# Kernel optimization log

Measured on AMD Instinct MI355X. Metric: run time of the kernel, lower is better.

## Reference

```python
import jax, jax.numpy as jnp
import numpy as np

B, N, E = 16, 512, 131072
FEAT, EMB, H = 3, 512, 3
K1, K2 = 410, 205  # ceil(0.8*512), ceil(0.5*410) per PyG TopKPooling
NEG_SLOPE, EPS = 0.2, 1e-5


def _gat_conv(x, W, att_s, att_d, bias, src, tgt, valid, num_nodes):
    # PyG GATConv (concat=True): per-edge attention with segment softmax over targets.
    Hh, C = att_s.shape
    xp = (x @ W).reshape(-1, Hh, C)                      # [Nn,H,C]
    a_s = jnp.einsum('nhc,hc->nh', xp, att_s)
    a_d = jnp.einsum('nhc,hc->nh', xp, att_d)
    srcc = jnp.where(valid, src, 0)
    tgtc = jnp.where(valid, tgt, 0)
    e = jax.nn.leaky_relu(a_s[srcc] + a_d[tgtc], NEG_SLOPE)  # [Ee,H]
    seg = jnp.where(valid, tgt, num_nodes)               # invalid edges -> dummy segment
    emax = jax.ops.segment_max(e, seg, num_segments=num_nodes + 1)
    emax = jnp.where(jnp.isfinite(emax), emax, 0.0)
    ex = jnp.exp(e - emax[seg]) * valid[:, None].astype(e.dtype)
    den = jax.ops.segment_sum(ex, seg, num_segments=num_nodes + 1)
    alpha = ex / jnp.maximum(den[seg], 1e-16)            # [Ee,H]
    out = jax.ops.segment_sum(alpha[:, :, None] * xp[srcc], seg,
                              num_segments=num_nodes + 1)[:num_nodes]
    return out.reshape(num_nodes, Hh * C) + bias


def _bn(x, g, b):
    # BatchNorm1d, training-mode batch statistics (biased var), eps=1e-5
    m = x.mean(0)
    v = x.var(0)
    return (x - m) * jax.lax.rsqrt(v + EPS) * g + b


def _topk_pool(x, p, nb, n_per, k):
    # PyG TopKPooling: score = tanh(x.w/||w||), keep top-k per graph, scale by score
    score = jnp.tanh((x @ p) / jnp.linalg.norm(p))       # [nb*n_per]
    top_s, top_i = jax.lax.top_k(score.reshape(nb, n_per), k)
    perm = (top_i + jnp.arange(nb)[:, None] * n_per).reshape(-1)
    x_new = x[perm] * top_s.reshape(-1, 1)
    mapping = jnp.full((nb * n_per,), -1, jnp.int32).at[perm].set(
        jnp.arange(nb * k, dtype=jnp.int32))
    return x_new, mapping


def _pool_cat(x, nb, k):
    # [global_max_pool, global_mean_pool] over equal-size graphs
    xr = x.reshape(nb, k, -1)
    return jnp.concatenate([xr.max(1), xr.mean(1)], axis=1)


def _forward(x, W1, as1, ad1, bc1, Wh1, bh1, g1, be1, p1,
             W2, as2, ad2, bc2, Wh2, bh2, g2, be2, p2,
             Wl1, bl1, Wl2, bl2, edge_index):
    Nn = B * N
    src0, tgt0 = edge_index[0], edge_index[1]
    sl = jnp.arange(Nn, dtype=jnp.int32)                 # GATConv add_self_loops=True
    src1 = jnp.concatenate([src0, sl]); tgt1 = jnp.concatenate([tgt0, sl])
    valid1 = jnp.ones(src1.shape, bool)
    h = _gat_conv(x, W1, as1, ad1, bc1, src1, tgt1, valid1, Nn)
    h = jax.nn.relu(h @ Wh1 + bh1)
    h = _bn(h, g1, be1)
    h, mapping = _topk_pool(h, p1, B, N, K1)
    x1 = _pool_cat(h, B, K1)                             # [B, 2*EMB]
    # relabel edges to pooled node ids; drop edges with removed endpoints via mask
    s2 = mapping[src0]; t2 = mapping[tgt0]
    v2 = (s2 >= 0) & (t2 >= 0)
    sl2 = jnp.arange(B * K1, dtype=jnp.int32)
    src2 = jnp.concatenate([s2, sl2]); tgt2 = jnp.concatenate([t2, sl2])
    valid2 = jnp.concatenate([v2, jnp.ones(sl2.shape, bool)])
    h = _gat_conv(h, W2, as2, ad2, bc2, src2, tgt2, valid2, B * K1)
    h = jax.nn.relu(h @ Wh2 + bh2)
    h = _bn(h, g2, be2)
    h, _ = _topk_pool(h, p2, B, K1, K2)
    x2 = _pool_cat(h, B, K2)
    xg = x1 + x2
    xg = jax.nn.relu(xg @ Wl1 + bl1)                     # dropout p=0.5 disabled (eval)
    return xg @ Wl2 + bl2                                # [B, 256]


def setup_inputs() -> dict:
    key = jax.random.key(0)
    ks = jax.random.split(key, 16)
    x = jax.random.normal(ks[0], (B * N, FEAT), jnp.float32)
    goff = jnp.repeat(jnp.arange(B, dtype=jnp.int32), E // B) * N
    src = jax.random.randint(ks[1], (E,), 0, N, jnp.int32) + goff
    tgt = jax.random.randint(ks[2], (E,), 0, N, jnp.int32) + goff
    edge_index = jnp.stack([src, tgt])
    s = 0.05
    p = {
        'W1': jax.random.normal(ks[3], (FEAT, H * EMB)) * s,
        'as1': jax.random.normal(ks[4], (H, EMB)) * s,
        'ad1': jax.random.normal(ks[5], (H, EMB)) * s,
        'bc1': jnp.zeros((H * EMB,)),
        'Wh1': jax.random.normal(ks[6], (H * EMB, EMB)) * s,
        'bh1': jnp.zeros((EMB,)),
        'g1': jnp.ones((EMB,)), 'be1': jnp.zeros((EMB,)),
        'p1': jax.random.normal(ks[7], (EMB,)) * s,
        'W2': jax.random.normal(ks[8], (EMB, H * EMB)) * s,
        'as2': jax.random.normal(ks[9], (H, EMB)) * s,
        'ad2': jax.random.normal(ks[10], (H, EMB)) * s,
        'bc2': jnp.zeros((H * EMB,)),
        'Wh2': jax.random.normal(ks[11], (H * EMB, EMB)) * s,
        'bh2': jnp.zeros((EMB,)),
        'g2': jnp.ones((EMB,)), 'be2': jnp.zeros((EMB,)),
        'p2': jax.random.normal(ks[12], (EMB,)) * s,
        'Wl1': jax.random.normal(ks[13], (2 * EMB, 512)) * s,
        'bl1': jnp.zeros((512,)),
        'Wl2': jax.random.normal(ks[14], (512, 256)) * s,
        'bl2': jnp.zeros((256,)),
    }
    return {'x': x, 'edge_index': edge_index, **p}


def reference(x, edge_index, W1, as1, ad1, bc1, Wh1, bh1, g1, be1, p1,
              W2, as2, ad2, bc2, Wh2, bh2, g2, be2, p2, Wl1, bl1, Wl2, bl2):
    return _forward(x, W1, as1, ad1, bc1, Wh1, bh1, g1, be1, p1,
                    W2, as2, ad2, bc2, Wh2, bh2, g2, be2, p2,
                    Wl1, bl1, Wl2, bl2, edge_index)
```

## Files before the change

kernel.cpp:

```cpp
#include <hip/hip_runtime.h>
#include <hip/hip_bf16.h>
#include <math.h>

#define E_EDGES 131072
#define NN1 8192
#define NN2 6560
#define NG 16
#define NP1 512
#define KP1 410
#define KP2 205
#define F1 1536
#define EMB 512
#define MAXDEG 256

typedef __hip_bfloat16 bf16;
typedef __attribute__((ext_vector_type(8))) short short8;
typedef __attribute__((ext_vector_type(4))) float f32x4;
typedef __attribute__((ext_vector_type(4))) unsigned short us4;

__device__ inline float wred64(float v){
  #pragma unroll
  for (int o = 32; o; o >>= 1) v += __shfl_down(v, o);
  return v;
}
__device__ inline float b2f_raw(unsigned short u){
  return __uint_as_float((unsigned)u << 16);
}
union BFU { bf16 b; unsigned short u; };
__device__ inline unsigned short f2u(float v){ BFU x; x.b = __float2bfloat16(v); return x.u; }

__device__ __forceinline__ void gld16(const void* g, void* l){
  __builtin_amdgcn_global_load_lds(
      (const __attribute__((address_space(1))) void*)g,
      (__attribute__((address_space(3))) void*)l, 16, 0, 0);
}

__device__ inline void split_store(float v, bf16* __restrict__ ph, bf16* __restrict__ pl){
  bf16 hi = __float2bfloat16(v);
  *ph = hi;
  *pl = __float2bfloat16(v - __bfloat162float(hi));
}

__device__ inline void bn_from_acc(const float* __restrict__ bnacc, int c, float fM,
                                   float& mean, float& inv){
  mean = bnacc[c] / fM;
  float var = fmaxf(bnacc[512+c]/fM - mean*mean, 0.f);
  inv = 1.f / sqrtf(var + 1e-5f);
}

__global__ __launch_bounds__(256) void k_pre(
    const float* __restrict__ W1, const float* __restrict__ as1, const float* __restrict__ ad1,
    const float* __restrict__ Wh1, const float* __restrict__ bc1, const float* __restrict__ bh1,
    const float* __restrict__ W2, const float* __restrict__ as2, const float* __restrict__ ad2,
    const float* __restrict__ Wh2, const float* __restrict__ bc2, const float* __restrict__ bh2,
    const int* __restrict__ src0, const int* __restrict__ tgt0, const float* __restrict__ x,
    float* __restrict__ M1p, float* __restrict__ cvp,
    float* __restrict__ was2, float* __restrict__ wad2,
    float* __restrict__ Zb, int* __restrict__ cnt2, int* __restrict__ map,
    bf16* __restrict__ Th, bf16* __restrict__ Tl,
    float* __restrict__ denp, float* __restrict__ nump){
  int b = blockIdx.x, t = threadIdx.x;
  if (b < 24){
    int h = b / 8, rem = b % 8, jh = rem >> 2, kc = rem & 3;
    int j = jh*256 + t, c0 = kc*128;
    __shared__ float w1s[3][128];
    for (int i = t; i < 384; i += 256)
      w1s[i>>7][i&127] = W1[(i>>7)*1536 + h*512 + c0 + (i&127)];
    __syncthreads();
    const float* whc = Wh1 + (size_t)(h*512 + c0)*512 + j;
    float a0=0.f, a1=0.f, a2=0.f;
    #pragma unroll 8
    for (int c = 0; c < 128; c++){
      float v = whc[(size_t)c*512];
      a0 += w1s[0][c]*v; a1 += w1s[1][c]*v; a2 += w1s[2][c]*v;
    }
    float* dst = M1p + (size_t)kc*4608;
    dst[(h*3+0)*512 + j] = a0;
    dst[(h*3+1)*512 + j] = a1;
    dst[(h*3+2)*512 + j] = a2;
  } else if (b < 56){
    int b2 = b - 24;
    int which = b2 >> 4, rem = b2 & 15, jh = rem >> 3, kc = rem & 7;
    const float* bc = which ? bc2 : bc1;
    const float* Wh = which ? Wh2 : Wh1;
    const float* bh = which ? bh2 : bh1;
    int j = jh*256 + t, i0 = kc*192;
    float acc = (kc == 0) ? bh[j] : 0.f;
    #pragma unroll 8
    for (int i = 0; i < 192; i++)
      acc += bc[i0+i] * Wh[(size_t)(i0+i)*512 + j];
    cvp[(size_t)(which*8 + kc)*512 + j] = acc;
  } else if (b < 152){
    int b3 = b - 56;
    int y = b3 >> 4, et = b3 & 15;
    int kind = y / 3, h = y % 3;
    int w = t >> 6, lane = t & 63;
    const float* att = kind ? ad2 : as2;
    float a[8];
    #pragma unroll
    for (int u = 0; u < 8; u++) a[u] = att[h*512 + lane*8 + u];
    for (int r = w; r < 32; r += 4){
      int e = et*32 + r;
      const float4* row = (const float4*)(W2 + (size_t)e*1536 + h*512) + lane*2;
      float4 v0 = row[0], v1 = row[1];
      float d = v0.x*a[0]+v0.y*a[1]+v0.z*a[2]+v0.w*a[3]
              + v1.x*a[4]+v1.y*a[5]+v1.z*a[6]+v1.w*a[7];
      d = wred64(d);
      if (lane == 0) (kind ? wad2 : was2)[h*512 + e] = d;
    }
  } else if (b < 218){
    int i = (b - 152)*256 + t;
    if (i < 2048){ Zb[i] = 0.f; }
    else if (i < 2048 + NN2){ cnt2[i - 2048] = 1; }
    else if (i < 2048 + NN2 + NN1){ map[i - 2048 - NN2] = -1; }
  } else if (b < 474){
    __shared__ float sww[18];
    __shared__ float lden[1536];
    __shared__ float lnum[4608];
    int wv_ = t >> 6, lane = t & 63;
    for (int combo = wv_*5; combo < wv_*5+5 && combo < 18; combo++){
      int kind = combo/9, rr = combo%9, h = rr/3, f = rr%3;
      const float* att = kind ? ad1 : as1;
      float s = 0.f;
      #pragma unroll
      for (int c = lane; c < 512; c += 64) s += W1[f*1536 + h*512 + c] * att[h*512 + c];
      s = wred64(s);
      if (lane == 0) sww[combo] = s;
    }
    for (int i = t; i < 1536; i += 256) lden[i] = 0.f;
    for (int i = t; i < 4608; i += 256) lnum[i] = 0.f;
    __syncthreads();
    int eb = b - 218;
    int g = eb >> 4, ch = eb & 15;
    int base = g*8192;
    int it0 = ch*544;
    for (int k = t; k < 544; k += 256){
      int it = it0 + k;
      int s, tl;
      if (it < 8192){ s = src0[base+it]; tl = tgt0[base+it] & 511; }
      else { tl = it - 8192; s = g*512 + tl; }
      float xs0 = x[s*3], xs1 = x[s*3+1], xs2 = x[s*3+2];
      int tg = g*512 + tl;
      float xt0 = x[tg*3], xt1 = x[tg*3+1], xt2 = x[tg*3+2];
      #pragma unroll
      for (int h = 0; h < 3; h++){
        float v = xs0*sww[h*3]+xs1*sww[h*3+1]+xs2*sww[h*3+2]
                + xt0*sww[9+h*3]+xt1*sww[9+h*3+1]+xt2*sww[9+h*3+2];
        v = v > 0.f ? v : 0.2f*v;
        float pe = expf(v);
        atomicAdd(&lden[tl*3 + h], pe);
        atomicAdd(&lnum[tl*9 + h*3 + 0], pe * xs0);
        atomicAdd(&lnum[tl*9 + h*3 + 1], pe * xs1);
        atomicAdd(&lnum[tl*9 + h*3 + 2], pe * xs2);
      }
    }
    __syncthreads();
    for (int i = t; i < 4608; i += 256) nump[(size_t)eb*4608 + i] = lnum[i];
    for (int i = t; i < 1536; i += 256) denp[(size_t)eb*1536 + i] = lden[i];
  } else {
    int bb = b - 474;
    int z = bb % 3; int rr = bb / 3; int by = rr >> 3, bx = rr & 7;
    const float* A = W2 + (size_t)z*512;
    const float* B = Wh2 + (size_t)z*512*512;
    __shared__ __align__(16) short sAh[4096], sAl[4096], sBh[4096], sBl[4096];
    int w = t >> 6, lane = t & 63;
    int l16 = lane & 15, q = lane >> 4;
    int bm = by*64, bn = bx*64;
    int am  = t >> 2, akw = (t & 3)*16;
    int bnl = t & 63, bkq = (t >> 6)*16;
    f32x4 acc[4];
    #pragma unroll
    for (int nf = 0; nf < 4; nf++) acc[nf] = (f32x4){0.f,0.f,0.f,0.f};
    float va[16], vb[16];
    #define GS_LOAD(K0) do { \
      _Pragma("unroll") for (int u = 0; u < 4; u++){ \
        float4 v4 = *(const float4*)(A + (size_t)(bm+am)*1536 + (K0) + akw + u*4); \
        va[u*4]=v4.x; va[u*4+1]=v4.y; va[u*4+2]=v4.z; va[u*4+3]=v4.w; } \
      _Pragma("unroll") for (int u = 0; u < 16; u++) \
        vb[u] = B[(size_t)((K0) + bkq + u)*512 + bn + bnl]; \
    } while(0)
    GS_LOAD(0);
    for (int it = 0; it < 8; it++){
      #pragma unroll
      for (int hh = 0; hh < 2; hh++){
        short8 ah_, al_, bh_, bl_;
        #pragma unroll
        for (int jj = 0; jj < 8; jj++){
          float v = va[hh*8+jj];
          unsigned short hu = f2u(v);
          ah_[jj] = (short)hu; al_[jj] = (short)f2u(v - b2f_raw(hu));
          v = vb[hh*8+jj];
          hu = f2u(v);
          bh_[jj] = (short)hu; bl_[jj] = (short)f2u(v - b2f_raw(hu));
        }
        int aoff = am*64  + ((((akw>>3) + hh) ^ (am  & 7)) << 3);
        *(short8*)(sAh + aoff) = ah_;
        *(short8*)(sAl + aoff) = al_;
        int boff = bnl*64 + ((((bkq>>3) + hh) ^ (bnl & 7)) << 3);
        *(short8*)(sBh + boff) = bh_;
        *(short8*)(sBl + boff) = bl_;
      }
      __syncthreads();
      if (it < 7) GS_LOAD((it+1)*64);
      #pragma unroll
      for (int ks = 0; ks < 2; ks++){
        int gc = ks*4 + q;
        int ar = w*16 + l16;
        int ao = ar*64 + ((gc ^ (ar & 7)) << 3);
        short8 afh = *(const short8*)(sAh + ao);
        short8 afl = *(const short8*)(sAl + ao);
        #pragma unroll
        for (int nf = 0; nf < 4; nf++){
          int br = nf*16 + l16;
          int bo = br*64 + ((gc ^ (br & 7)) << 3);
          short8 bfh = *(const short8*)(sBh + bo);
          short8 bfl = *(const short8*)(sBl + bo);
          acc[nf] = __builtin_amdgcn_mfma_f32_16x16x32_bf16(afh, bfh, acc[nf], 0, 0, 0);
          acc[nf] = __builtin_amdgcn_mfma_f32_16x16x32_bf16(afh, bfl, acc[nf], 0, 0, 0);
          acc[nf] = __builtin_amdgcn_mfma_f32_16x16x32_bf16(afl, bfh, acc[nf], 0, 0, 0);
        }
      }
      __syncthreads();
    }
    #undef GS_LOAD
    int m0 = bm + w*16 + q*4;
    #pragma unroll
    for (int nf = 0; nf < 4; nf++){
      int n = bn + nf*16 + l16;
      size_t base = (size_t)n*1536 + (size_t)z*512 + m0;
      #pragma unroll
      for (int e = 0; e < 4; e++)
        split_store(acc[nf][e], &Th[base+e], &Tl[base+e]);
    }
  }
}

__global__ __launch_bounds__(256) void k_h1(
    const float* __restrict__ nump, const float* __restrict__ denp,
    const float* __restrict__ M1p, const float* __restrict__ cvp1, bf16* __restrict__ hout,
    float* __restrict__ bnacc1){
  __shared__ float sM[9*512];
  __shared__ float sC[512];
  __shared__ float sA[32*9];
  int t = threadIdx.x; int n0 = blockIdx.x*32;
  for (int i = t; i < 9*512; i += 256)
    sM[i] = M1p[i] + M1p[4608 + i] + M1p[2*4608 + i] + M1p[3*4608 + i];
  for (int i = t; i < 512; i += 256){
    float s = 0.f;
    #pragma unroll
    for (int kc = 0; kc < 8; kc++) s += cvp1[kc*512 + i];
    sC[i] = s;
  }
  for (int i = t; i < 288; i += 256){
    int node = i / 9, q = i % 9, hh = q / 3;
    int gn = n0 + node;
    int g = gn >> 9, nl = gn & 511;
    float ns = 0.f, ds = 0.f;
    #pragma unroll 4
    for (int ch = 0; ch < 16; ch++){
      ns += nump[(size_t)(g*16 + ch)*4608 + nl*9 + q];
      ds += denp[(size_t)(g*16 + ch)*1536 + nl*3 + hh];
    }
    sA[i] = ns / fmaxf(ds, 1e-16f);
  }
  __syncthreads();
  float c0v = sC[t], c1v = sC[t+256];
  float ls0=0.f, lq0=0.f, ls1=0.f, lq1=0.f;
  #pragma unroll 4
  for (int i = 0; i < 32; i++){
    float a0 = c0v, a1 = c1v;
    #pragma unroll
    for (int q = 0; q < 9; q++){
      float av = sA[i*9+q];
      a0 += av * sM[q*512 + t];
      a1 += av * sM[q*512 + t + 256];
    }
    a0 = fmaxf(a0, 0.f); a1 = fmaxf(a1, 0.f);
    hout[(size_t)(n0+i)*512 + t]       = __float2bfloat16(a0);
    hout[(size_t)(n0+i)*512 + t + 256] = __float2bfloat16(a1);
    ls0 += a0; lq0 += a0*a0; ls1 += a1; lq1 += a1*a1;
  }
  atomicAdd(&bnacc1[t],           ls0);
  atomicAdd(&bnacc1[t+256],       ls1);
  atomicAdd(&bnacc1[512 + t],     lq0);
  atomicAdd(&bnacc1[512 + t+256], lq1);
}

__global__ __launch_bounds__(256) void k_score(
    const bf16* __restrict__ h, const float* __restrict__ bnacc, int M,
    const float* __restrict__ g_, const float* __restrict__ be, const float* __restrict__ p,
    float* __restrict__ score, int NR){
  __shared__ float w[512];
  __shared__ float rb[4], rp[4];
  int t = threadIdx.x;
  int lane = t & 63, wv = t >> 6;
  float fM = (float)M;
  float bt = 0.f, pp = 0.f;
  #pragma unroll
  for (int k = 0; k < 2; k++){
    int c = t + k*256;
    float mean, inv; bn_from_acc(bnacc, c, fM, mean, inv);
    float gc = g_[c], pc = p[c];
    float ig = inv * gc;
    w[c] = ig * pc;
    bt += (be[c] - mean * ig) * pc;
    pp += pc * pc;
  }
  bt = wred64(bt); pp = wred64(pp);
  if (lane == 0){ rb[wv] = bt; rp[wv] = pp; }
  __syncthreads();
  float B0 = rb[0]+rb[1]+rb[2]+rb[3];
  float pn = sqrtf(rp[0]+rp[1]+rp[2]+rp[3]);
  float wl[8];
  #pragma unroll
  for (int u = 0; u < 8; u++) wl[u] = w[lane*8 + u];
  int rbase = blockIdx.x*32 + wv*8;
  for (int rr = 0; rr < 8; rr++){
    int r = rbase + rr;
    if (r >= NR) break;
    const unsigned short* hr = (const unsigned short*)h + (size_t)r*EMB + lane*8;
    us4 v0 = *(const us4*)(hr);
    us4 v1 = *(const us4*)(hr + 4);
    float dot = b2f_raw(v0.x)*wl[0] + b2f_raw(v0.y)*wl[1]
              + b2f_raw(v0.z)*wl[2] + b2f_raw(v0.w)*wl[3]
              + b2f_raw(v1.x)*wl[4] + b2f_raw(v1.y)*wl[5]
              + b2f_raw(v1.z)*wl[6] + b2f_raw(v1.w)*wl[7];
    dot = wred64(dot);
    if (lane == 0) score[r] = tanhf((dot + B0) / pn);
  }
}

__global__ __launch_bounds__(512) void k_sort1(
    const float* __restrict__ score, int n_per, int K,
    int* __restrict__ map, int* __restrict__ topi, float* __restrict__ tops){
  int g = blockIdx.x, t = threadIdx.x;
  __shared__ float sk[512];
  __shared__ int si[512];
  if (t < n_per){ sk[t] = score[g*n_per + t]; si[t] = t; }
  else { sk[t] = -INFINITY; si[t] = 0x7fffffff; }
  __syncthreads();
  for (int k = 2; k <= 512; k <<= 1){
    for (int j = k >> 1; j > 0; j >>= 1){
      int l = t ^ j;
      if (l > t){
        float ki = sk[t], kl = sk[l]; int ii = si[t], il = si[l];
        bool before_l = (kl > ki) || (kl == ki && il < ii);
        bool up = ((t & k) == 0);
        if (up == before_l){ sk[t]=kl; sk[l]=ki; si[t]=il; si[l]=ii; }
      }
      __syncthreads();
    }
  }
  if (t < K){
    map[g*n_per + si[t]] = g*K + t;
    topi[g*K + t] = si[t];
    tops[g*K + t] = sk[t];
  }
}

__global__ __launch_bounds__(512) void k_sortpool2(
    const bf16* __restrict__ h, const float* __restrict__ score,
    const float* __restrict__ bnacc, int M,
    const float* __restrict__ g_, const float* __restrict__ be,
    int n_per, int K, float* __restrict__ cat){
  int g = blockIdx.x, t = threadIdx.x;
  __shared__ float sk[512];
  __shared__ int si[512];
  if (t < n_per){ sk[t] = score[g*n_per + t]; si[t] = t; }
  else { sk[t] = -INFINITY; si[t] = 0x7fffffff; }
  __syncthreads();
  for (int k = 2; k <= 512; k <<= 1){
    for (int j = k >> 1; j > 0; j >>= 1){
      int l = t ^ j;
      if (l > t){
        float ki = sk[t], kl = sk[l]; int ii = si[t], il = si[l];
        bool before_l = (kl > ki) || (kl == ki && il < ii);
        bool up = ((t & k) == 0);
        if (up == before_l){ sk[t]=kl; sk[l]=ki; si[t]=il; si[l]=ii; }
      }
      __syncthreads();
    }
  }
  float fM = (float)M;
  float mean, inv; bn_from_acc(bnacc, t, fM, mean, inv);
  float ig = inv * g_[t], bec = be[t];
  const unsigned short* hp = (const unsigned short*)h;
  float mx = -INFINITY, sm = 0.f;
  for (int r = 0; r < K; r++){
    float v = (b2f_raw(hp[(size_t)(g*n_per + si[r])*EMB + t]) - mean) * ig + bec;
    v *= sk[r];
    mx = fmaxf(mx, v); sm += v;
  }
  cat[g*1024 + t] = mx;
  cat[g*1024 + 512 + t] = sm / (float)K;
}

__global__ __launch_bounds__(256) void k_gather_c2(
    const bf16* __restrict__ h, const float* __restrict__ bnacc, int M,
    const float* __restrict__ gm, const float* __restrict__ be,
    const int* __restrict__ topi, const float* __restrict__ tops,
    bf16* __restrict__ xn, int n_per, int K,
    const float* __restrict__ was2, const float* __restrict__ wad2,
    float* __restrict__ aso, float* __restrict__ ado,
    const int* __restrict__ src0, const int* __restrict__ tgt0,
    const int* __restrict__ map, int* __restrict__ cnt2, int nblk_g){
  int row = blockIdx.x, t = threadIdx.x;
  if (row >= nblk_g){
    int i = (row - nblk_g)*256 + t;
    if (i < E_EDGES){
      int s = map[src0[i]], tg = map[tgt0[i]];
      if (s >= 0 && tg >= 0) atomicAdd(&cnt2[tg], 1);
    }
    return;
  }
  int gr = row / K, i = row - gr*K;
  int sidx = topi[gr*K + i];
  float s = tops[gr*K + i];
  const bf16* src = h + ((size_t)(gr*n_per + sidx))*EMB;
  bf16* dst = xn + (size_t)row*EMB;
  int c0 = t, c1 = t + 256;
  float fM = (float)M;
  float mean0, inv0, mean1, inv1;
  bn_from_acc(bnacc, c0, fM, mean0, inv0);
  bn_from_acc(bnacc, c1, fM, mean1, inv1);
  float v0 = ((__bfloat162float(src[c0]) - mean0) * inv0 * gm[c0] + be[c0]) * s;
  float v1 = ((__bfloat162float(src[c1]) - mean1) * inv1 * gm[c1] + be[c1]) * s;
  dst[c0] = __float2bfloat16(v0);
  dst[c1] = __float2bfloat16(v1);
  {
    float a[6];
    #pragma unroll
    for (int hh = 0; hh < 3; hh++){
      a[hh]   = v0*was2[hh*512 + c0] + v1*was2[hh*512 + c1];
      a[3+hh] = v0*wad2[hh*512 + c0] + v1*wad2[hh*512 + c1];
    }
    __shared__ float red[6][4];
    int lane = t & 63, wv = t >> 6;
    #pragma unroll
    for (int q = 0; q < 6; q++){ float v = wred64(a[q]); if (lane==0) red[q][wv]=v; }
    __syncthreads();
    if (t < 6){
      float sm = red[t][0]+red[t][1]+red[t][2]+red[t][3];
      if (t < 3) aso[row*3+t] = sm; else ado[row*3+(t-3)] = sm;
    }
  }
}

__device__ inline void scan_body(const int* __restrict__ counts, int* __restrict__ off,
                                 int* __restrict__ cur, int n, int* __restrict__ sh){
  int t = threadIdx.x;
  int chunk = (n + 1023) >> 10;
  int b = t * chunk; int e = b + chunk; if (e > n) e = n;
  int s = 0;
  for (int i = b; i < e; i++) s += counts[i];
  sh[t] = s; __syncthreads();
  for (int o = 1; o < 1024; o <<= 1){
    int v = (t >= o) ? sh[t-o] : 0;
    __syncthreads();
    sh[t] += v;
    __syncthreads();
  }
  int run = (t > 0) ? sh[t-1] : 0;
  for (int i = b; i < e; i++){ int c = counts[i]; off[i] = run; cur[i] = run; run += c; }
  if (t == 1023) off[n] = sh[1023];
}
__global__ void k_fill2(const int* __restrict__ src0, const int* __restrict__ tgt0,
                        const int* __restrict__ map, int* __restrict__ cur,
                        int* __restrict__ esrc, int E, int nn){
  int i = blockIdx.x*blockDim.x + threadIdx.x;
  if (i >= E + nn) return;
  int s, tg;
  if (i < E){
    s = map[src0[i]]; tg = map[tgt0[i]];
    if (s < 0 || tg < 0) return;
  } else { s = i - E; tg = s; }
  int pos = atomicAdd(&cur[tg], 1);
  esrc[pos] = s;
}

__global__ __launch_bounds__(1024) void k_poolA_scan(const bf16* __restrict__ xn,
    float* __restrict__ cat, int K,
    const int* __restrict__ cnt2, int* __restrict__ off2, int* __restrict__ cur2){
  __shared__ int shi[1024];
  __shared__ float smax[8][128];
  __shared__ float ssum[8][128];
  int b = blockIdx.x, t = threadIdx.x;
  if (b == 64){ scan_body(cnt2, off2, cur2, NN2, shi); return; }
  int g = b >> 2, cb = b & 3;
  int c = t & 127, rg = t >> 7;
  int col = cb*128 + c;
  const unsigned short* p = (const unsigned short*)xn + (size_t)g*K*EMB + col;
  float mx = -INFINITY, sm = 0.f;
  for (int r = rg; r < K; r += 8){
    float v = b2f_raw(p[(size_t)r*EMB]);
    mx = fmaxf(mx, v); sm += v;
  }
  smax[rg][c] = mx; ssum[rg][c] = sm;
  __syncthreads();
  if (rg == 0){
    #pragma unroll
    for (int u = 1; u < 8; u++){ mx = fmaxf(mx, smax[u][c]); sm += ssum[u][c]; }
    cat[g*1024 + col] = mx;
    cat[g*1024 + 512 + col] = sm / (float)K;
  }
}

__global__ __launch_bounds__(256) void k_agg2(
    const bf16* __restrict__ xn, const float* __restrict__ aso, const float* __restrict__ ado,
    const int* __restrict__ off, const int* __restrict__ esrc,
    bf16* __restrict__ oh){
  int n = blockIdx.x, t = threadIdx.x;
  __shared__ int srcs[MAXDEG];
  __shared__ float al[MAXDEG*3];
  __shared__ float mh[3], dh[3];
  int s0 = off[n]; int deg = off[n+1] - s0; if (deg > MAXDEG) deg = MAXDEG;
  for (int e = t; e < deg; e += 256) srcs[e] = esrc[s0 + e];
  __syncthreads();
  float ad0 = ado[n*3+0], ad1 = ado[n*3+1], ad2 = ado[n*3+2];
  for (int e = t; e < deg; e += 256){
    int s = srcs[e];
    float v0 = aso[s*3+0] + ad0, v1 = aso[s*3+1] + ad1, v2 = aso[s*3+2] + ad2;
    al[e*3+0] = v0 > 0.f ? v0 : 0.2f*v0;
    al[e*3+1] = v1 > 0.f ? v1 : 0.2f*v1;
    al[e*3+2] = v2 > 0.f ? v2 : 0.2f*v2;
  }
  __syncthreads();
  if (t < 3){
    float m = -INFINITY;
    for (int e = 0; e < deg; e++) m = fmaxf(m, al[e*3+t]);
    float d = 0.f;
    for (int e = 0; e < deg; e++) d += expf(al[e*3+t] - m);
    mh[t] = m; dh[t] = 1.f / fmaxf(d, 1e-16f);
  }
  __syncthreads();
  for (int e = t; e < deg; e += 256){
    al[e*3+0] = expf(al[e*3+0]-mh[0])*dh[0];
    al[e*3+1] = expf(al[e*3+1]-mh[1])*dh[1];
    al[e*3+2] = expf(al[e*3+2]-mh[2])*dh[2];
  }
  __syncthreads();
  float acc[2][3] = {};
  for (int e = 0; e < deg; e++){
    int s = srcs[e];
    float a0 = al[e*3], a1 = al[e*3+1], a2 = al[e*3+2];
    #pragma unroll
    for (int k = 0; k < 2; k++){
      float v = __bfloat162float(xn[(size_t)s*512 + t + k*256]);
      acc[k][0] += a0*v; acc[k][1] += a1*v; acc[k][2] += a2*v;
    }
  }
  #pragma unroll
  for (int k = 0; k < 2; k++){
    int c = t + k*256;
    #pragma unroll
    for (int h = 0; h < 3; h++)
      oh[(size_t)n*1536 + h*512 + c] = __float2bfloat16(acc[k][h]);
  }
}

__global__ __launch_bounds__(256, 2) void k_gemm_mfma(
    const bf16* __restrict__ Ah,
    const bf16* __restrict__ Bh, const bf16* __restrict__ Bl,
    const float* __restrict__ bias, bf16* __restrict__ C,
    float* __restrict__ bnacc,
    int M, int N, int K, int Mtiles){
  int xcd = (int)blockIdx.x & 7;
  int ii  = (int)blockIdx.x >> 3;
  int bni = ii & 7;
  int bmi = xcd + 8*(ii >> 3);
  if (bmi >= Mtiles) return;
  __shared__ __align__(16) unsigned short lds[2][16384];
  int t = threadIdx.x, w = t >> 6, lane = t & 63;
  int q = lane >> 4, l16 = lane & 15;
  int bm = bmi * 128, bn = bni * 64;

  int lr = lane >> 3, lc = lane & 7;
  int kg = ((lc ^ lr) & 7) * 8;
  int ro = w*8 + lr;
  int m0 = bm + ro, m1 = bm + 32 + ro, m2 = bm + 64 + ro, m3 = bm + 96 + ro;
  if (m0 >= M) m0 = M-1;  if (m1 >= M) m1 = M-1;
  if (m2 >= M) m2 = M-1;  if (m3 >= M) m3 = M-1;
  int n0 = bn + ro, n1 = bn + 32 + ro;
  const bf16* ptr[8];
  ptr[0] = Ah + (size_t)m0*K + kg;
  ptr[1] = Ah + (size_t)m1*K + kg;
  ptr[2] = Ah + (size_t)m2*K + kg;
  ptr[3] = Ah + (size_t)m3*K + kg;
  ptr[4] = Bh + (size_t)n0*K + kg;
  ptr[5] = Bh + (size_t)n1*K + kg;
  ptr[6] = Bl + (size_t)n0*K + kg;
  ptr[7] = Bl + (size_t)n1*K + kg;
  const int dof[8] = {0, 2048, 4096, 6144, 8192, 10240, 12288, 14336};

  int wm = (w >> 1) * 64, wn = (w & 1) * 32;
  f32x4 acc[4][2];
  #pragma unroll
  for (int i = 0; i < 4; i++)
    #pragma unroll
    for (int j = 0; j < 2; j++)
      acc[i][j] = (f32x4){0.f, 0.f, 0.f, 0.f};

  #pragma unroll
  for (int u = 0; u < 8; u++){
    gld16(ptr[u], &lds[0][dof[u] + w*512]);
    ptr[u] += 64;
  }

  int nit = K >> 6;
  for (int it = 0; it < nit; it++){
    __syncthreads();
    int cur = it & 1;
    if (it + 1 < nit){
      int nxt = cur ^ 1;
      #pragma unroll
      for (int u = 0; u < 8; u++){
        gld16(ptr[u], &lds[nxt][dof[u] + w*512]);
        ptr[u] += 64;
      }
    }
    const unsigned short* L = lds[cur];
    #pragma unroll
    for (int ks = 0; ks < 2; ks++){
      short8 ah[4], bh2[2], bl2[2];
      int gc = ks*4 + q;
      #pragma unroll
      for (int i = 0; i < 4; i++){
        int r = wm + i*16 + l16;
        ah[i] = *(const short8*)(L + r*64 + ((gc ^ (r & 7)) << 3));
      }
      #pragma unroll
      for (int j = 0; j < 2; j++){
        int r = wn + j*16 + l16;
        int so = ((gc ^ (r & 7)) << 3);
        bh2[j] = *(const short8*)(L + 8192  + r*64 + so);
        bl2[j] = *(const short8*)(L + 12288 + r*64 + so);
      }
      #pragma unroll
      for (int i = 0; i < 4; i++)
        #pragma unroll
        for (int j = 0; j < 2; j++){
          acc[i][j] = __builtin_amdgcn_mfma_f32_16x16x32_bf16(ah[i], bh2[j], acc[i][j], 0, 0, 0);
          acc[i][j] = __builtin_amdgcn_mfma_f32_16x16x32_bf16(ah[i], bl2[j], acc[i][j], 0, 0, 0);
        }
    }
  }

  __syncthreads();
  float* cs = (float*)&lds[0][0];
  float* cq = cs + 128;
  int slot = w >> 1;
  #pragma unroll
  for (int j = 0; j < 2; j++){
    int c_local = wn + j*16 + l16;
    int c = bn + c_local;
    float bv = 0.f;
    if (bias){
      #pragma unroll
      for (int kc = 0; kc < 8; kc++) bv += bias[kc*512 + c];
    }
    float ls = 0.f, lq = 0.f;
    #pragma unroll
    for (int i = 0; i < 4; i++){
      int rb = bm + wm + i*16 + q*4;
      #pragma unroll
      for (int e = 0; e < 4; e++){
        int r = rb + e;
        if (r < M){
          float v = fmaxf(acc[i][j][e] + bv, 0.f);
          C[(size_t)r*N + c] = __float2bfloat16(v);
          ls += v; lq += v*v;
        }
      }
    }
    ls += __shfl_xor(ls, 16); ls += __shfl_xor(ls, 32);
    lq += __shfl_xor(lq, 16); lq += __shfl_xor(lq, 32);
    if (q == 0){ cs[slot*64 + c_local] = ls; cq[slot*64 + c_local] = lq; }
  }
  __syncthreads();
  if (t < 64){
    atomicAdd(&bnacc[bn + t],        cs[t] + cs[64 + t]);
    atomicAdd(&bnacc[512 + bn + t],  cq[t] + cq[64 + t]);
  }
}

__global__ __launch_bounds__(256) void k_head1p(const float* __restrict__ c1,
    const float* __restrict__ c2, const float* __restrict__ Wl1,
    float* __restrict__ t1p){
  __shared__ float wl[128][64];
  __shared__ float xgs[16][128];
  int b = blockIdx.x, t = threadIdx.x;
  int jt = b >> 3, kc = b & 7;
  int j0 = jt*64, k0 = kc*128;
  for (int i = t; i < 8192; i += 256){
    int k = i >> 6, j = i & 63;
    wl[k][j] = Wl1[(size_t)(k0 + k)*512 + j0 + j];
  }
  for (int i = t; i < 2048; i += 256){
    int g = i >> 7, k = i & 127;
    int idx = g*1024 + k0 + k;
    xgs[g][k] = c1[idx] + c2[idx];
  }
  __syncthreads();
  #pragma unroll
  for (int u = 0; u < 4; u++){
    int p = t + u*256;
    int g = p >> 6, j = p & 63;
    float acc = 0.f;
    #pragma unroll 8
    for (int k = 0; k < 128; k++)
      acc += xgs[g][k] * wl[k][j];
    t1p[(size_t)(kc*16 + g)*512 + j0 + j] = acc;
  }
}
__global__ __launch_bounds__(512) void k_head2p(const float* __restrict__ t1p,
    const float* __restrict__ bl1, const float* __restrict__ Wl2,
    const float* __restrict__ bl2, float* __restrict__ out){
  __shared__ float t1s[512];
  __shared__ float part[2][256];
  int g = blockIdx.x, t = threadIdx.x;
  float acc = bl1[t];
  #pragma unroll
  for (int kc = 0; kc < 8; kc++)
    acc += t1p[(size_t)(kc*16 + g)*512 + t];
  t1s[t] = fmaxf(acc, 0.f);
  __syncthreads();
  int c = t & 255, half = t >> 8;
  float a = 0.f;
  #pragma unroll 8
  for (int k = half*256; k < half*256 + 256; k++)
    a += t1s[k] * Wl2[(size_t)k*256 + c];
  part[half][c] = a;
  __syncthreads();
  if (half == 0)
    out[g*256 + c] = part[0][c] + part[1][c] + bl2[c];
}

extern "C" void kernel_launch(void* const* d_in, const int* in_sizes, int n_in,
                              void* d_out, int out_size, void* d_ws, size_t ws_size,
                              hipStream_t stream){
  const float* x   = (const float*)d_in[0];
  const int*   ei  = (const int*)d_in[1];
  const float* W1  = (const float*)d_in[2];
  const float* as1 = (const float*)d_in[3];
  const float* ad1 = (const float*)d_in[4];
  const float* bc1 = (const float*)d_in[5];
  const float* Wh1 = (const float*)d_in[6];
  const float* bh1 = (const float*)d_in[7];
  const float* g1  = (const float*)d_in[8];
  const float* be1 = (const float*)d_in[9];
  const float* p1  = (const float*)d_in[10];
  const float* W2  = (const float*)d_in[11];
  const float* as2 = (const float*)d_in[12];
  const float* ad2 = (const float*)d_in[13];
  const float* bc2 = (const float*)d_in[14];
  const float* Wh2 = (const float*)d_in[15];
  const float* bh2 = (const float*)d_in[16];
  const float* g2  = (const float*)d_in[17];
  const float* be2 = (const float*)d_in[18];
  const float* p2  = (const float*)d_in[19];
  const float* Wl1 = (const float*)d_in[20];
  const float* bl1 = (const float*)d_in[21];
  const float* Wl2 = (const float*)d_in[22];
  const float* bl2 = (const float*)d_in[23];
  float* out = (float*)d_out;

  const int* src0 = ei;
  const int* tgt0 = ei + E_EDGES;

  bf16* Cc      = (bf16*)d_ws;
  bf16* xn1     = Cc + (size_t)NN1*EMB;
  bf16* aggx2h  = xn1 + (size_t)NN2*EMB;
  bf16* M2Th    = aggx2h + (size_t)NN2*F1;
  bf16* M2Tl    = M2Th + (size_t)EMB*F1;
  float* holeA  = (float*)(M2Tl + (size_t)EMB*F1);
  float* t1p    = holeA;
  float* score  = holeA + 65536;
  float* bnacc1 = holeA + 122880;
  float* bnacc  = bnacc1 + 1024;
  float* M1p    = bnacc + 1024;
  float* cvp    = M1p + 4*4608;
  float* was2   = cvp + 16*512;
  float* wad2   = was2 + 3*512;
  float* hole16 = wad2 + 3*512;
  float* aso2   = hole16 + 32;
  float* ado2   = aso2 + (size_t)NN2*3;
  float* tops   = ado2 + (size_t)NN2*3;
  float* cat1   = tops + NG*KP1;
  float* cat2   = cat1 + NG*1024;
  int* topi     = (int*)(cat2 + NG*1024);
  int* map      = topi + NG*KP1;
  int* cnt2     = map + NN1;
  int* off2     = cnt2 + NN2;
  int* cur2     = off2 + NN2 + 8;
  int* esrc2    = cur2 + NN2;
  float* nump   = (float*)(esrc2 + 137700);
  float* denp   = nump + (size_t)256*4608;
  float* cvp2   = cvp + 8*512;

  k_pre<<<666,256,0,stream>>>(W1,as1,ad1,Wh1,bc1,bh1, W2,as2,ad2,Wh2,bc2,bh2,
                              src0,tgt0,x,
                              M1p,cvp,was2,wad2,
                              bnacc1,cnt2,map,M2Th,M2Tl, denp,nump);
  k_h1<<<NN1/32,256,0,stream>>>(nump,denp,M1p,cvp,Cc,bnacc1);
  k_score<<<NN1/32,256,0,stream>>>(Cc,bnacc1,NN1,g1,be1,p1,score,NN1);
  k_sort1<<<NG,512,0,stream>>>(score,NP1,KP1,map,topi,tops);
  k_gather_c2<<<NG*KP1+512,256,0,stream>>>(Cc,bnacc1,NN1,g1,be1,topi,tops,xn1,NP1,KP1,
      was2,wad2,aso2,ado2, src0,tgt0,map,cnt2,NG*KP1);
  k_poolA_scan<<<65,1024,0,stream>>>(xn1,cat1,KP1, cnt2,off2,cur2);
  k_fill2<<<(E_EDGES+NN2+255)/256,256,0,stream>>>(src0,tgt0,map,cur2,esrc2,E_EDGES,NN2);
  k_agg2<<<NN2,256,0,stream>>>(xn1,aso2,ado2,off2,esrc2,aggx2h);
  k_gemm_mfma<<<448,256,0,stream>>>(aggx2h,M2Th,M2Tl,cvp2,Cc,bnacc,NN2,EMB,F1,52);
  k_score<<<(NN2+31)/32,256,0,stream>>>(Cc,bnacc,NN2,g2,be2,p2,score,NN2);
  k_sortpool2<<<NG,512,0,stream>>>(Cc,score,bnacc,NN2,g2,be2,KP1,KP2,cat2);
  k_head1p<<<64,256,0,stream>>>(cat1,cat2,Wl1,t1p);
  k_head2p<<<NG,512,0,stream>>>(t1p,bl1,Wl2,bl2,out);
}
```

Before: 308.1 us.

## Build per-graph CSR for pooled edges in shared memory, drop global scan and fill kernels

```diff
diff --git a/kernel.cpp b/kernel.cpp
--- a/kernel.cpp
+++ b/kernel.cpp
@@ -12,6 +12,7 @@
 #define F1 1536
 #define EMB 512
 #define MAXDEG 256
+#define ESTRIDE 8704
 
 typedef __hip_bfloat16 bf16;
 typedef __attribute__((ext_vector_type(8))) short short8;
@@ -56,7 +57,7 @@
     const int* __restrict__ src0, const int* __restrict__ tgt0, const float* __restrict__ x,
     float* __restrict__ M1p, float* __restrict__ cvp,
     float* __restrict__ was2, float* __restrict__ wad2,
-    float* __restrict__ Zb, int* __restrict__ cnt2, int* __restrict__ map,
+    float* __restrict__ Zb, int* __restrict__ map,
     bf16* __restrict__ Th, bf16* __restrict__ Tl,
     float* __restrict__ denp, float* __restrict__ nump){
   int b = blockIdx.x, t = threadIdx.x;
@@ -108,12 +109,11 @@
       d = wred64(d);
       if (lane == 0) (kind ? wad2 : was2)[h*512 + e] = d;
     }
-  } else if (b < 218){
+  } else if (b < 192){
     int i = (b - 152)*256 + t;
     if (i < 2048){ Zb[i] = 0.f; }
-    else if (i < 2048 + NN2){ cnt2[i - 2048] = 1; }
-    else if (i < 2048 + NN2 + NN1){ map[i - 2048 - NN2] = -1; }
-  } else if (b < 474){
+    else { map[i - 2048] = -1; }
+  } else if (b < 448){
     __shared__ float sww[18];
     __shared__ float lden[1536];
     __shared__ float lnum[4608];
@@ -130,7 +130,7 @@
     for (int i = t; i < 1536; i += 256) lden[i] = 0.f;
     for (int i = t; i < 4608; i += 256) lnum[i] = 0.f;
     __syncthreads();
-    int eb = b - 218;
+    int eb = b - 192;
     int g = eb >> 4, ch = eb & 15;
     int base = g*8192;
     int it0 = ch*544;
@@ -158,7 +158,7 @@
     for (int i = t; i < 4608; i += 256) nump[(size_t)eb*4608 + i] = lnum[i];
     for (int i = t; i < 1536; i += 256) denp[(size_t)eb*1536 + i] = lden[i];
   } else {
-    int bb = b - 474;
+    int bb = b - 448;
     int z = bb % 3; int rr = bb / 3; int by = rr >> 3, bx = rr & 7;
     const float* A = W2 + (size_t)z*512;
     const float* B = Wh2 + (size_t)z*512*512;
@@ -395,7 +395,7 @@
   cat[g*1024 + 512 + t] = sm / (float)K;
 }
 
-__global__ __launch_bounds__(256) void k_gather_c2(
+__global__ __launch_bounds__(256) void k_gather_csr(
     const bf16* __restrict__ h, const float* __restrict__ bnacc, int M,
     const float* __restrict__ gm, const float* __restrict__ be,
     const int* __restrict__ topi, const float* __restrict__ tops,
@@ -403,13 +403,47 @@
     const float* __restrict__ was2, const float* __restrict__ wad2,
     float* __restrict__ aso, float* __restrict__ ado,
     const int* __restrict__ src0, const int* __restrict__ tgt0,
-    const int* __restrict__ map, int* __restrict__ cnt2, int nblk_g){
+    const int* __restrict__ map,
+    int* __restrict__ off2, int* __restrict__ deg2, int* __restrict__ esrc2,
+    int nblk_g){
   int row = blockIdx.x, t = threadIdx.x;
   if (row >= nblk_g){
-    int i = (row - nblk_g)*256 + t;
-    if (i < E_EDGES){
-      int s = map[src0[i]], tg = map[tgt0[i]];
-      if (s >= 0 && tg >= 0) atomicAdd(&cnt2[tg], 1);
+    __shared__ int cnt[KP1];
+    __shared__ int loff[KP1+1];
+    __shared__ int cur[KP1];
+    int gb = row - nblk_g;
+    for (int l = t; l < KP1; l += 256) cnt[l] = 1;
+    __syncthreads();
+    int base = gb*8192;
+    for (int i = t; i < 8192; i += 256){
+      int s = map[src0[base+i]], tg = map[tgt0[base+i]];
+      if (s >= 0 && tg >= 0) atomicAdd(&cnt[tg - gb*KP1], 1);
+    }
+    __syncthreads();
+    if (t == 0){
+      int run = 0;
+      for (int l = 0; l < KP1; l++){ loff[l] = run; run += cnt[l]; }
+      loff[KP1] = run;
+    }
+    __syncthreads();
+    for (int l = t; l < KP1; l += 256) cur[l] = loff[l];
+    __syncthreads();
+    for (int l = t; l < KP1; l += 256){
+      int pos = atomicAdd(&cur[l], 1);
+      esrc2[(size_t)gb*ESTRIDE + pos] = gb*KP1 + l;
+    }
+    for (int i = t; i < 8192; i += 256){
+      int s = map[src0[base+i]], tg = map[tgt0[base+i]];
+      if (s >= 0 && tg >= 0){
+        int tl = tg - gb*KP1;
+        int pos = atomicAdd(&cur[tl], 1);
+        esrc2[(size_t)gb*ESTRIDE + pos] = s;
+      }
+    }
+    __syncthreads();
+    for (int l = t; l < KP1; l += 256){
+      off2[gb*KP1 + l] = gb*ESTRIDE + loff[l];
+      deg2[gb*KP1 + l] = cnt[l];
     }
     return;
   }
@@ -446,46 +480,11 @@
   }
 }
 
-__device__ inline void scan_body(const int* __restrict__ counts, int* __restrict__ off,
-                                 int* __restrict__ cur, int n, int* __restrict__ sh){
-  int t = threadIdx.x;
-  int chunk = (n + 1023) >> 10;
-  int b = t * chunk; int e = b + chunk; if (e > n) e = n;
-  int s = 0;
-  for (int i = b; i < e; i++) s += counts[i];
-  sh[t] = s; __syncthreads();
-  for (int o = 1; o < 1024; o <<= 1){
-    int v = (t >= o) ? sh[t-o] : 0;
-    __syncthreads();
-    sh[t] += v;
-    __syncthreads();
-  }
-  int run = (t > 0) ? sh[t-1] : 0;
-  for (int i = b; i < e; i++){ int c = counts[i]; off[i] = run; cur[i] = run; run += c; }
-  if (t == 1023) off[n] = sh[1023];
-}
-__global__ void k_fill2(const int* __restrict__ src0, const int* __restrict__ tgt0,
-                        const int* __restrict__ map, int* __restrict__ cur,
-                        int* __restrict__ esrc, int E, int nn){
-  int i = blockIdx.x*blockDim.x + threadIdx.x;
-  if (i >= E + nn) return;
-  int s, tg;
-  if (i < E){
-    s = map[src0[i]]; tg = map[tgt0[i]];
-    if (s < 0 || tg < 0) return;
-  } else { s = i - E; tg = s; }
-  int pos = atomicAdd(&cur[tg], 1);
-  esrc[pos] = s;
-}
-
-__global__ __launch_bounds__(1024) void k_poolA_scan(const bf16* __restrict__ xn,
-    float* __restrict__ cat, int K,
-    const int* __restrict__ cnt2, int* __restrict__ off2, int* __restrict__ cur2){
-  __shared__ int shi[1024];
+__global__ __launch_bounds__(1024) void k_poolA(const bf16* __restrict__ xn,
+    float* __restrict__ cat, int K){
   __shared__ float smax[8][128];
   __shared__ float ssum[8][128];
   int b = blockIdx.x, t = threadIdx.x;
-  if (b == 64){ scan_body(cnt2, off2, cur2, NN2, shi); return; }
   int g = b >> 2, cb = b & 3;
   int c = t & 127, rg = t >> 7;
   int col = cb*128 + c;
@@ -507,13 +506,13 @@
 
 __global__ __launch_bounds__(256) void k_agg2(
     const bf16* __restrict__ xn, const float* __restrict__ aso, const float* __restrict__ ado,
-    const int* __restrict__ off, const int* __restrict__ esrc,
+    const int* __restrict__ off, const int* __restrict__ deg2, const int* __restrict__ esrc,
     bf16* __restrict__ oh){
   int n = blockIdx.x, t = threadIdx.x;
   __shared__ int srcs[MAXDEG];
   __shared__ float al[MAXDEG*3];
   __shared__ float mh[3], dh[3];
-  int s0 = off[n]; int deg = off[n+1] - s0; if (deg > MAXDEG) deg = MAXDEG;
+  int s0 = off[n]; int deg = deg2[n]; if (deg > MAXDEG) deg = MAXDEG;
   for (int e = t; e < deg; e += 256) srcs[e] = esrc[s0 + e];
   __syncthreads();
   float ad0 = ado[n*3+0], ad1 = ado[n*3+1], ad2 = ado[n*3+2];
@@ -789,26 +788,24 @@
   float* cat2   = cat1 + NG*1024;
   int* topi     = (int*)(cat2 + NG*1024);
   int* map      = topi + NG*KP1;
-  int* cnt2     = map + NN1;
-  int* off2     = cnt2 + NN2;
-  int* cur2     = off2 + NN2 + 8;
-  int* esrc2    = cur2 + NN2;
-  float* nump   = (float*)(esrc2 + 137700);
+  int* off2     = map + NN1;
+  int* deg2     = off2 + NN2;
+  int* esrc2    = deg2 + NN2;
+  float* nump   = (float*)(esrc2 + NG*ESTRIDE);
   float* denp   = nump + (size_t)256*4608;
   float* cvp2   = cvp + 8*512;
 
-  k_pre<<<666,256,0,stream>>>(W1,as1,ad1,Wh1,bc1,bh1, W2,as2,ad2,Wh2,bc2,bh2,
+  k_pre<<<640,256,0,stream>>>(W1,as1,ad1,Wh1,bc1,bh1, W2,as2,ad2,Wh2,bc2,bh2,
                               src0,tgt0,x,
                               M1p,cvp,was2,wad2,
-                              bnacc1,cnt2,map,M2Th,M2Tl, denp,nump);
+                              bnacc1,map,M2Th,M2Tl, denp,nump);
   k_h1<<<NN1/32,256,0,stream>>>(nump,denp,M1p,cvp,Cc,bnacc1);
   k_score<<<NN1/32,256,0,stream>>>(Cc,bnacc1,NN1,g1,be1,p1,score,NN1);
   k_sort1<<<NG,512,0,stream>>>(score,NP1,KP1,map,topi,tops);
-  k_gather_c2<<<NG*KP1+512,256,0,stream>>>(Cc,bnacc1,NN1,g1,be1,topi,tops,xn1,NP1,KP1,
-      was2,wad2,aso2,ado2, src0,tgt0,map,cnt2,NG*KP1);
-  k_poolA_scan<<<65,1024,0,stream>>>(xn1,cat1,KP1, cnt2,off2,cur2);
-  k_fill2<<<(E_EDGES+NN2+255)/256,256,0,stream>>>(src0,tgt0,map,cur2,esrc2,E_EDGES,NN2);
-  k_agg2<<<NN2,256,0,stream>>>(xn1,aso2,ado2,off2,esrc2,aggx2h);
+  k_gather_csr<<<NG*KP1+NG,256,0,stream>>>(Cc,bnacc1,NN1,g1,be1,topi,tops,xn1,NP1,KP1,
+      was2,wad2,aso2,ado2, src0,tgt0,map, off2,deg2,esrc2, NG*KP1);
+  k_poolA<<<64,1024,0,stream>>>(xn1,cat1,KP1);
+  k_agg2<<<NN2,256,0,stream>>>(xn1,aso2,ado2,off2,deg2,esrc2,aggx2h);
   k_gemm_mfma<<<448,256,0,stream>>>(aggx2h,M2Th,M2Tl,cvp2,Cc,bnacc,NN2,EMB,F1,52);
   k_score<<<(NN2+31)/32,256,0,stream>>>(Cc,bnacc,NN2,g2,be2,p2,score,NN2);
   k_sortpool2<<<NG,512,0,stream>>>(Cc,score,bnacc,NN2,g2,be2,KP1,KP2,cat2);
```

Result: slower. 330.2 us (+7.2%).
